# Optimization experiments

Measured on AMD Instinct MI355X. Metric: run time of the kernel, lower is better.

Reference implementation:

```python
import jax, jax.numpy as jnp
import numpy as np

B, S, D, N = 4, 2048, 256, 12  # batch, seq_len, hidden_size(=size_per_head), heads


def setup_inputs() -> dict:
    key = jax.random.key(0)
    k1, k2, k3, k4, k5 = jax.random.split(key, 5)
    std = 0.02
    return {
        "input_tensor": jax.random.normal(k1, (B, S, D), dtype=jnp.float32),
        "attention_mask": jnp.ones((B, S, S), dtype=jnp.int32),
        "qk_kernel": jax.random.normal(k2, (D, N, D), dtype=jnp.float32) * std,
        "qk_bias": jnp.zeros((N, D), dtype=jnp.float32),
        "v_kernel": jax.random.normal(k3, (D, N, D), dtype=jnp.float32) * std,
        "v_bias": jnp.zeros((N, D), dtype=jnp.float32),
    }


def reference(input_tensor, attention_mask, qk_kernel, qk_bias, v_kernel, v_bias):
    # Dense3D projections: [B,F,D_in] x [D_in,N,D] -> [B,F,N,D]
    query_key = jnp.einsum('bfc,cnd->bfnd', input_tensor, qk_kernel) + qk_bias
    value = jnp.einsum('bfc,cnd->bfnd', input_tensor, v_kernel) + v_bias
    # scores[b,n,s,f] = sum_d query_key[b,f,n,d] * input_tensor[b,s,d]
    # (original broadcasts input over heads; broadcasting is implicit here)
    scores = jnp.einsum('bfnd,bsd->bnsf', query_key, input_tensor)
    adder = (1.0 - attention_mask.astype(scores.dtype)) * -10000.0  # [B,S,F]
    scores = scores + adder[:, None, :, :]  # broadcast over heads
    probs = jax.nn.softmax(scores, axis=-1)  # softmax over F
    # dropout rate is 0.0 -> identity
    # context [B,S,N,D] then sum over heads -> fuse into one einsum [B,S,D]
    out = jnp.einsum('bnsf,bfnd->bsd', probs, value)
    return out
```

## Files before the change

kernel.cpp:

```cpp
#include <hip/hip_runtime.h>
#include <stdint.h>

#define B_ 4
#define S_ 2048
#define D_ 256
#define NH_ 12
#define M_ (B_*S_)
#define J_ (NH_*D_)

typedef __bf16 bf16;
typedef __bf16 bf16x8 __attribute__((ext_vector_type(8)));
typedef __bf16 bf16x4 __attribute__((ext_vector_type(4)));
typedef float  f32x4  __attribute__((ext_vector_type(4)));

#define MFMA16(a,b,c) __builtin_amdgcn_mfma_f32_16x16x32_bf16(a,b,c,0,0,0)

__device__ __forceinline__ void g2lds16(void* l, const void* g) {
  __builtin_amdgcn_global_load_lds(
      (const __attribute__((address_space(1))) unsigned int*)g,
      (__attribute__((address_space(3))) unsigned int*)l, 16, 0, 0);
}

__global__ __launch_bounds__(256) void cvt_x(const float* __restrict__ in,
                                             bf16* __restrict__ out) {
  int i = blockIdx.x * 256 + threadIdx.x;
  f32x4 v = *(const f32x4*)(in + (size_t)i * 4);
  bf16x4 o;
#pragma unroll
  for (int k = 0; k < 4; ++k) o[k] = (bf16)v[k];
  *(bf16x4*)(out + (size_t)i * 4) = o;
}

__global__ __launch_bounds__(256) void transpose_w(const float* __restrict__ W0,
                                                   bf16* __restrict__ T0,
                                                   const float* __restrict__ W1,
                                                   bf16* __restrict__ T1) {
  const float* W = blockIdx.z ? W1 : W0;
  bf16* Wt       = blockIdx.z ? T1 : T0;
  int j  = blockIdx.x * 256 + threadIdx.x;
  int c0 = blockIdx.y * 16;
  bf16x8 v0, v1;
#pragma unroll
  for (int i = 0; i < 8; ++i) v0[i] = (bf16)W[(size_t)(c0 + i) * J_ + j];
#pragma unroll
  for (int i = 0; i < 8; ++i) v1[i] = (bf16)W[(size_t)(c0 + 8 + i) * J_ + j];
  *(bf16x8*)(Wt + (size_t)j * D_ + c0)     = v0;
  *(bf16x8*)(Wt + (size_t)j * D_ + c0 + 8) = v1;
}

__global__ __launch_bounds__(256) void mask_flags_k(const int* __restrict__ mask,
                                                    int* __restrict__ flags) {
  int bx = blockIdx.x;
  int ft = bx & 31, st = (bx >> 5) & 31, b = bx >> 10;
  int t = threadIdx.x;
  const int4* mp4 = (const int4*)(mask + (size_t)b * S_ * S_ +
                                  (size_t)(st * 64 + (t >> 2)) * S_ + ft * 64 + (t & 3) * 16);
  bool ok = true;
#pragma unroll
  for (int i = 0; i < 4; ++i) {
    int4 v = mp4[i];
    ok &= (v.x == 1) & (v.y == 1) & (v.z == 1) & (v.w == 1);
  }
  __shared__ int flag;
  if (t == 0) flag = 1;
  __syncthreads();
  if (!ok) flag = 0;
  __syncthreads();
  if (t == 0) flags[bx] = flag;
}

__device__ __forceinline__ void gemm_body(
    const bf16* __restrict__ A, const bf16* __restrict__ Bm,
    const float* __restrict__ bias, bf16* __restrict__ C,
    int Ndim, int bias_mode, int bid)
{
  __shared__ bf16 As[128 * 64];
  __shared__ bf16 Bs[128 * 64];
  const int nbn = Ndim >> 7;
  const int bm = bid / nbn, bn = bid % nbn;
  const int t = threadIdx.x, w = t >> 6, l = t & 63;
  const int lane16 = l & 15, quad = l >> 4;
  const int wm = (w & 1) << 6, wn = (w >> 1) << 6;
  const int srow = t >> 3;
  const int gc = (t & 7) ^ (srow & 7);
  const bf16* Ag = A + (size_t)((bm << 7) + srow) * 256 + gc * 8;
  const bf16* Bg = Bm + (size_t)((bn << 7) + srow) * 256 + gc * 8;
  f32x4 acc[4][4] = {};
  for (int k0 = 0; k0 < 256; k0 += 64) {
    __syncthreads();
#pragma unroll
    for (int i = 0; i < 4; ++i)
      g2lds16(As + (size_t)(i * 256 + (w << 6)) * 8, Ag + (size_t)i * 32 * 256 + k0);
#pragma unroll
    for (int i = 0; i < 4; ++i)
      g2lds16(Bs + (size_t)(i * 256 + (w << 6)) * 8, Bg + (size_t)i * 32 * 256 + k0);
    __syncthreads();
#pragma unroll
    for (int kt = 0; kt < 2; ++kt) {
      bf16x8 af[4], bfr[4];
#pragma unroll
      for (int i = 0; i < 4; ++i)
        af[i] = *(const bf16x8*)(As + (wm + i * 16 + lane16) * 64 +
                                 (((kt * 4 + quad) ^ (lane16 & 7)) * 8));
#pragma unroll
      for (int i = 0; i < 4; ++i)
        bfr[i] = *(const bf16x8*)(Bs + (wn + i * 16 + lane16) * 64 +
                                  (((kt * 4 + quad) ^ (lane16 & 7)) * 8));
#pragma unroll
      for (int i = 0; i < 4; ++i)
#pragma unroll
        for (int jx = 0; jx < 4; ++jx)
          acc[i][jx] = MFMA16(af[i], bfr[jx], acc[i][jx]);
    }
  }
#pragma unroll
  for (int i = 0; i < 4; ++i)
#pragma unroll
    for (int jx = 0; jx < 4; ++jx) {
      int col = (bn << 7) + wn + jx * 16 + lane16;
#pragma unroll
      for (int r = 0; r < 4; ++r) {
        int row = (bm << 7) + wm + i * 16 + quad * 4 + r;
        float v = acc[i][jx][r] + (bias_mode ? bias[row] : bias[col]);
        C[(size_t)row * Ndim + col] = (bf16)v;
      }
    }
}

__global__ __launch_bounds__(256) void gemm_both(
    const bf16* __restrict__ Xbf, const bf16* __restrict__ Wqkt,
    const float* __restrict__ bqk, bf16* __restrict__ QKw,
    const bf16* __restrict__ Wvt, const float* __restrict__ bv,
    bf16* __restrict__ Vtw)
{
  int bid = blockIdx.x;
  if (bid < 1536) gemm_body(Xbf, Wqkt, bqk, QKw, J_, 0, bid);
  else            gemm_body(Wvt, Xbf, bv, Vtw, M_, 1, bid - 1536);
}

__global__ __launch_bounds__(256, 2) void attn_k(
    const bf16* __restrict__ X, const bf16* __restrict__ QK, const bf16* __restrict__ Vt,
    const int* __restrict__ mask, const int* __restrict__ flags,
    bf16* __restrict__ Ctx)
{
  __shared__ bf16 Ks[2][32 * 256];
  __shared__ bf16 Vs[2][256 * 32];
  __shared__ bf16 Ps[4][32 * 40];
  const int i  = blockIdx.x;
  const int x  = i & 7, rr = i >> 3;
  const int g  = x + 8 * (rr >> 4);
  const int st = rr & 15;
  const int b  = g / 12, n = g % 12;
  const int t = threadIdx.x, w = t >> 6, l = t & 63;
  const int lane16 = l & 15, quad = l >> 4;
  const int sw = (st << 7) + (w << 5);
  const bf16* Xb = X + (size_t)b * S_ * D_;
  bf16x8 qf[2][8];
#pragma unroll
  for (int ts = 0; ts < 2; ++ts)
#pragma unroll
    for (int kt = 0; kt < 8; ++kt)
      qf[ts][kt] = *(const bf16x8*)(Xb + (size_t)(sw + ts * 16 + lane16) * D_ + kt * 32 + quad * 8);
  const bf16* QKb = QK + (size_t)b * S_ * J_ + n * D_;
  const bf16* Vtb = Vt + (size_t)n * D_ * M_ + (size_t)b * S_;
  const int* flagb = flags + (b * 32 + st * 2 + (w >> 1)) * 32;
  f32x4 oacc[2][16] = {};
  float lsum[2] = {0.f, 0.f};

  auto stage = [&](int buf, int f0) {
#pragma unroll
    for (int ii = 0; ii < 4; ++ii) {
      int frow = ii * 8 + (t >> 5);
      int dc = (t & 31) ^ (frow & 7);
      g2lds16(&Ks[buf][ii * 2048 + (w << 9)], QKb + (size_t)(f0 + frow) * J_ + dc * 8);
    }
#pragma unroll
    for (int ii = 0; ii < 4; ++ii) {
      int drow = ii * 64 + (t >> 2);
      int fc = (t & 3) ^ ((drow >> 1) & 3);
      g2lds16(&Vs[buf][ii * 2048 + (w << 9)], Vtb + (size_t)drow * M_ + f0 + fc * 8);
    }
  };

  stage(0, 0);
  int cur = 0;
  for (int f0 = 0; f0 < S_; f0 += 32) {
    __syncthreads();
    if (f0 + 32 < S_) stage(cur ^ 1, f0 + 32);
    f32x4 sfr[2][2] = {};
#pragma unroll
    for (int kt = 0; kt < 8; ++kt)
#pragma unroll
      for (int ct = 0; ct < 2; ++ct) {
        int fl = ct * 16 + lane16;
        bf16x8 kf = *(const bf16x8*)(&Ks[cur][fl * 256 + (((kt * 4 + quad) ^ (fl & 7)) * 8)]);
        sfr[0][ct] = MFMA16(kf, qf[0][kt], sfr[0][ct]);
        sfr[1][ct] = MFMA16(kf, qf[1][kt], sfr[1][ct]);
      }
    float ex[2][2][4];
    if (flagb[f0 >> 6]) {
#pragma unroll
      for (int ts = 0; ts < 2; ++ts)
#pragma unroll
        for (int ct = 0; ct < 2; ++ct)
#pragma unroll
          for (int r = 0; r < 4; ++r) ex[ts][ct][r] = __expf(sfr[ts][ct][r]);
    } else {
#pragma unroll
      for (int ts = 0; ts < 2; ++ts)
#pragma unroll
        for (int ct = 0; ct < 2; ++ct)
#pragma unroll
          for (int r = 0; r < 4; ++r) {
            int s = sw + ts * 16 + lane16, f = f0 + ct * 16 + quad * 4 + r;
            float add = (1.0f - (float)mask[(size_t)b * S_ * S_ + (size_t)s * S_ + f]) * -10000.0f;
            ex[ts][ct][r] = __expf(sfr[ts][ct][r] + add);
          }
    }
#pragma unroll
    for (int ts = 0; ts < 2; ++ts)
      lsum[ts] += ex[ts][0][0] + ex[ts][0][1] + ex[ts][0][2] + ex[ts][0][3]
                + ex[ts][1][0] + ex[ts][1][1] + ex[ts][1][2] + ex[ts][1][3];
#pragma unroll
    for (int ts = 0; ts < 2; ++ts)
#pragma unroll
      for (int ct = 0; ct < 2; ++ct) {
        int base = (ts * 16 + lane16) * 40 + ct * 16 + quad * 4;
        bf16x4 pv;
        pv[0] = (bf16)ex[ts][ct][0]; pv[1] = (bf16)ex[ts][ct][1];
        pv[2] = (bf16)ex[ts][ct][2]; pv[3] = (bf16)ex[ts][ct][3];
        *(bf16x4*)(&Ps[w][base]) = pv;
      }
    bf16x8 pf[2];
#pragma unroll
    for (int ts = 0; ts < 2; ++ts)
      pf[ts] = *(const bf16x8*)(&Ps[w][(ts * 16 + lane16) * 40 + quad * 8]);
#pragma unroll
    for (int dt = 0; dt < 16; ++dt) {
      int dl = dt * 16 + lane16;
      bf16x8 vf = *(const bf16x8*)(&Vs[cur][dl * 32 + ((quad ^ ((dl >> 1) & 3)) * 8)]);
      oacc[0][dt] = MFMA16(pf[0], vf, oacc[0][dt]);
      oacc[1][dt] = MFMA16(pf[1], vf, oacc[1][dt]);
    }
    cur ^= 1;
  }
  float tot[2];
#pragma unroll
  for (int ts = 0; ts < 2; ++ts) {
    float rs = lsum[ts];
    rs += __shfl_xor(rs, 16);
    rs += __shfl_xor(rs, 32);
    tot[ts] = rs;
  }
  bf16* Cb = Ctx + (size_t)(b * NH_ + n) * S_ * D_;
#pragma unroll
  for (int ts = 0; ts < 2; ++ts)
#pragma unroll
    for (int r = 0; r < 4; ++r) {
      float inv = 1.0f / __shfl(tot[ts], quad * 4 + r, 16);
      int s = sw + ts * 16 + quad * 4 + r;
#pragma unroll
      for (int dt = 0; dt < 16; ++dt) {
        int d = dt * 16 + lane16;
        Cb[(size_t)s * D_ + d] = (bf16)(oacc[ts][dt][r] * inv);
      }
    }
}

__global__ __launch_bounds__(256) void head_sum(const bf16* __restrict__ Ctx,
                                                float* __restrict__ out) {
  int i = blockIdx.x * 256 + threadIdx.x;
  int m = i >> 5;
  int dc = (i & 31) * 8;
  int b = m >> 11, s = m & 2047;
  const bf16* p = Ctx + ((size_t)(b * NH_) * S_ + s) * D_ + dc;
  float acc[8] = {};
#pragma unroll
  for (int n = 0; n < NH_; ++n) {
    bf16x8 v = *(const bf16x8*)(p + (size_t)n * S_ * D_);
#pragma unroll
    for (int k = 0; k < 8; ++k) acc[k] += (float)v[k];
  }
  f32x4 o0, o1;
#pragma unroll
  for (int k = 0; k < 4; ++k) { o0[k] = acc[k]; o1[k] = acc[4 + k]; }
  float* q = out + (size_t)m * D_ + dc;
  *(f32x4*)q = o0;
  *(f32x4*)(q + 4) = o1;
}

extern "C" void kernel_launch(void* const* d_in, const int* in_sizes, int n_in,
                              void* d_out, int out_size, void* d_ws, size_t ws_size,
                              hipStream_t stream) {
  (void)in_sizes; (void)n_in; (void)out_size; (void)ws_size;
  const float* X    = (const float*)d_in[0];
  const int*   mask = (const int*)d_in[1];
  const float* Wqk  = (const float*)d_in[2];
  const float* bqk  = (const float*)d_in[3];
  const float* Wv   = (const float*)d_in[4];
  const float* bv   = (const float*)d_in[5];
  float* out = (float*)d_out;

  char* p = (char*)d_ws;
  bf16*  Xbf  = (bf16*)p;  p += (size_t)M_ * D_ * 2;
  bf16*  Wqkt = (bf16*)p;  p += (size_t)J_ * D_ * 2;
  bf16*  Wvt  = (bf16*)p;  p += (size_t)J_ * D_ * 2;
  bf16*  QKw  = (bf16*)p;  p += (size_t)M_ * J_ * 2;
  bf16*  Vtw  = (bf16*)p;  p += (size_t)J_ * M_ * 2;
  bf16*  Ctx  = (bf16*)p;  p += (size_t)B_ * NH_ * S_ * D_ * 2;
  int*   flags= (int*)p;   p += 4096 * 4;

  cvt_x<<<(M_ * D_) / (256 * 4), 256, 0, stream>>>(X, Xbf);
  transpose_w<<<dim3(12, 16, 2), 256, 0, stream>>>(Wqk, Wqkt, Wv, Wvt);
  mask_flags_k<<<4096, 256, 0, stream>>>(mask, flags);
  gemm_both<<<3072, 256, 0, stream>>>(Xbf, Wqkt, bqk, QKw, Wvt, bv, Vtw);
  attn_k<<<B_ * NH_ * (S_ / 128), 256, 0, stream>>>(Xbf, QKw, Vtw, mask, flags, Ctx);
  head_sum<<<(M_ * D_ / 8) / 256, 256, 0, stream>>>(Ctx, out);
}
```

Before: 454.4 us.

## Split attention over key dimension into two halves with deferred normalization

The attention kernel now optionally splits the F (key) loop into two halves, doubling the grid from 768 to 1536 blocks so more CUs are busy. Each half writes unnormalized partial context and row sums, and head_sum combines both halves and normalizes while summing over heads. This is possible because the softmax uses no max subtraction, so partial sums simply add. The cost is twice the partial-context traffic through global memory and a larger workspace requirement. It falls back to a single pass if the workspace is too small.

```diff
diff --git a/kernel.cpp b/kernel.cpp
--- a/kernel.cpp
+++ b/kernel.cpp
@@ -138,19 +138,24 @@
   else            gemm_body(Wvt, Xbf, bv, Vtw, M_, 1, bid - 1536);
 }
 
+template<int HS>
 __global__ __launch_bounds__(256, 2) void attn_k(
     const bf16* __restrict__ X, const bf16* __restrict__ QK, const bf16* __restrict__ Vt,
     const int* __restrict__ mask, const int* __restrict__ flags,
-    bf16* __restrict__ Ctx)
+    bf16* __restrict__ Part, float* __restrict__ Lsum)
 {
   __shared__ bf16 Ks[2][32 * 256];
   __shared__ bf16 Vs[2][256 * 32];
   __shared__ bf16 Ps[4][32 * 40];
   const int i  = blockIdx.x;
   const int x  = i & 7, rr = i >> 3;
-  const int g  = x + 8 * (rr >> 4);
+  const int gh = x + 8 * (rr >> 4);
   const int st = rr & 15;
+  const int h  = HS ? (gh >= 48 ? 1 : 0) : 0;
+  const int g  = gh - 48 * h;
   const int b  = g / 12, n = g % 12;
+  const int f_beg = h * 1024;
+  const int f_end = f_beg + (HS ? 1024 : 2048);
   const int t = threadIdx.x, w = t >> 6, l = t & 63;
   const int lane16 = l & 15, quad = l >> 4;
   const int sw = (st << 7) + (w << 5);
@@ -182,11 +187,11 @@
     }
   };
 
-  stage(0, 0);
+  stage(0, f_beg);
   int cur = 0;
-  for (int f0 = 0; f0 < S_; f0 += 32) {
+  for (int f0 = f_beg; f0 < f_end; f0 += 32) {
     __syncthreads();
-    if (f0 + 32 < S_) stage(cur ^ 1, f0 + 32);
+    if (f0 + 32 < f_end) stage(cur ^ 1, f0 + 32);
     f32x4 sfr[2][2] = {};
 #pragma unroll
     for (int kt = 0; kt < 8; ++kt)
@@ -252,34 +257,52 @@
     rs += __shfl_xor(rs, 32);
     tot[ts] = rs;
   }
-  bf16* Cb = Ctx + (size_t)(b * NH_ + n) * S_ * D_;
+  bf16*  Cb = Part + (size_t)(h * 48 + g) * S_ * D_;
+  float* Lb = Lsum + (size_t)(h * 48 + g) * S_;
+  if (l < 16) {
+#pragma unroll
+    for (int ts = 0; ts < 2; ++ts) Lb[sw + ts * 16 + l] = tot[ts];
+  }
 #pragma unroll
   for (int ts = 0; ts < 2; ++ts)
 #pragma unroll
     for (int r = 0; r < 4; ++r) {
-      float inv = 1.0f / __shfl(tot[ts], quad * 4 + r, 16);
       int s = sw + ts * 16 + quad * 4 + r;
 #pragma unroll
       for (int dt = 0; dt < 16; ++dt) {
         int d = dt * 16 + lane16;
-        Cb[(size_t)s * D_ + d] = (bf16)(oacc[ts][dt][r] * inv);
+        Cb[(size_t)s * D_ + d] = (bf16)oacc[ts][dt][r];
       }
     }
 }
 
-__global__ __launch_bounds__(256) void head_sum(const bf16* __restrict__ Ctx,
+template<int HS>
+__global__ __launch_bounds__(256) void head_sum(const bf16* __restrict__ Part,
+                                                const float* __restrict__ Lsum,
                                                 float* __restrict__ out) {
   int i = blockIdx.x * 256 + threadIdx.x;
   int m = i >> 5;
   int dc = (i & 31) * 8;
   int b = m >> 11, s = m & 2047;
-  const bf16* p = Ctx + ((size_t)(b * NH_) * S_ + s) * D_ + dc;
   float acc[8] = {};
 #pragma unroll
   for (int n = 0; n < NH_; ++n) {
-    bf16x8 v = *(const bf16x8*)(p + (size_t)n * S_ * D_);
-#pragma unroll
-    for (int k = 0; k < 8; ++k) acc[k] += (float)v[k];
+    int g = b * NH_ + n;
+    const bf16* p = Part + ((size_t)g * S_ + s) * D_ + dc;
+    float lv = Lsum[(size_t)g * S_ + s];
+    bf16x8 v0 = *(const bf16x8*)p;
+    float a[8];
+#pragma unroll
+    for (int k = 0; k < 8; ++k) a[k] = (float)v0[k];
+    if (HS) {
+      lv += Lsum[(size_t)(48 + g) * S_ + s];
+      bf16x8 v1 = *(const bf16x8*)(p + (size_t)48 * S_ * D_);
+#pragma unroll
+      for (int k = 0; k < 8; ++k) a[k] += (float)v1[k];
+    }
+    float inv = 1.0f / lv;
+#pragma unroll
+    for (int k = 0; k < 8; ++k) acc[k] += a[k] * inv;
   }
   f32x4 o0, o1;
 #pragma unroll
@@ -292,7 +315,7 @@
 extern "C" void kernel_launch(void* const* d_in, const int* in_sizes, int n_in,
                               void* d_out, int out_size, void* d_ws, size_t ws_size,
                               hipStream_t stream) {
-  (void)in_sizes; (void)n_in; (void)out_size; (void)ws_size;
+  (void)in_sizes; (void)n_in; (void)out_size;
   const float* X    = (const float*)d_in[0];
   const int*   mask = (const int*)d_in[1];
   const float* Wqk  = (const float*)d_in[2];
@@ -307,13 +330,21 @@
   bf16*  Wvt  = (bf16*)p;  p += (size_t)J_ * D_ * 2;
   bf16*  QKw  = (bf16*)p;  p += (size_t)M_ * J_ * 2;
   bf16*  Vtw  = (bf16*)p;  p += (size_t)J_ * M_ * 2;
-  bf16*  Ctx  = (bf16*)p;  p += (size_t)B_ * NH_ * S_ * D_ * 2;
   int*   flags= (int*)p;   p += 4096 * 4;
+  float* Lsum = (float*)p; p += (size_t)2 * 48 * S_ * 4;
+  bf16*  Part = (bf16*)p;
+  size_t need = (size_t)(p - (char*)d_ws) + (size_t)2 * 48 * S_ * D_ * 2;
+  int hs = (ws_size >= need) ? 1 : 0;
 
   cvt_x<<<(M_ * D_) / (256 * 4), 256, 0, stream>>>(X, Xbf);
   transpose_w<<<dim3(12, 16, 2), 256, 0, stream>>>(Wqk, Wqkt, Wv, Wvt);
   mask_flags_k<<<4096, 256, 0, stream>>>(mask, flags);
   gemm_both<<<3072, 256, 0, stream>>>(Xbf, Wqkt, bqk, QKw, Wvt, bv, Vtw);
-  attn_k<<<B_ * NH_ * (S_ / 128), 256, 0, stream>>>(Xbf, QKw, Vtw, mask, flags, Ctx);
-  head_sum<<<(M_ * D_ / 8) / 256, 256, 0, stream>>>(Ctx, out);
-}
+  if (hs) {
+    attn_k<1><<<B_ * NH_ * (S_ / 128) * 2, 256, 0, stream>>>(Xbf, QKw, Vtw, mask, flags, Part, Lsum);
+    head_sum<1><<<(M_ * D_ / 8) / 256, 256, 0, stream>>>(Part, Lsum, out);
+  } else {
+    attn_k<0><<<B_ * NH_ * (S_ / 128), 256, 0, stream>>>(Xbf, QKw, Vtw, mask, flags, Part, Lsum);
+    head_sum<0><<<(M_ * D_ / 8) / 256, 256, 0, stream>>>(Part, Lsum, out);
+  }
+}
```

After: 453.8 us. About the same (-0.1%).
